# Optimization experiments

Measured on AMD Instinct MI355X. Metric: run time of the kernel, lower is better.

Reference implementation:

```python
import jax, jax.numpy as jnp
import numpy as np

DIM = 512
NUM_HEADS = 8
HEAD_DIM = DIM // NUM_HEADS
GAMMA = 1.0


def setup_inputs() -> dict:
    key = jax.random.key(0)
    ks = jax.random.split(key, 10)
    B, S = 2, 2048
    x_real = jax.random.normal(ks[0], (B, S, DIM), dtype=jnp.float32)
    x_imag = jax.random.normal(ks[1], (B, S, DIM), dtype=jnp.float32)
    def xavier(k, fan_in, fan_out):
        lim = float(np.sqrt(6.0 / (fan_in + fan_out)))
        return jax.random.uniform(k, (fan_in, fan_out), jnp.float32, -lim, lim)
    # torch Linear(in,out): weight [out,in]; we store transposed [in,out]
    Wq = xavier(ks[2], 2 * DIM, DIM); bq = jnp.zeros((DIM,), jnp.float32)
    Wk = xavier(ks[3], 2 * DIM, DIM); bk = jnp.zeros((DIM,), jnp.float32)
    Wv = xavier(ks[4], 2 * DIM, DIM); bv = jnp.zeros((DIM,), jnp.float32)
    Wo = xavier(ks[5], DIM, 2 * DIM); bo = jnp.zeros((2 * DIM,), jnp.float32)
    return {"x_real": x_real, "x_imag": x_imag, "Wq": Wq, "bq": bq,
            "Wk": Wk, "bk": bk, "Wv": Wv, "bv": bv, "Wo": Wo, "bo": bo}


def reference(x_real, x_imag, Wq, bq, Wk, bk, Wv, bv, Wo, bo):
    B, S, _ = x_real.shape
    real_embed = jnp.concatenate([x_real, x_imag], axis=-1)  # [B,S,2*dim]
    def proj(W, b):
        y = real_embed @ W + b                               # [B,S,dim]
        return y.reshape(B, S, NUM_HEADS, HEAD_DIM).transpose(0, 2, 1, 3)  # [B,H,S,d]
    Q = proj(Wq, bq)
    K = proj(Wk, bk)
    V = proj(Wv, bv)
    # softmax over head_dim is broadcast-invariant, so the Bhattacharyya
    # coefficient sum_d sqrt(p_i[d]*q_j[d]) factorizes into a matmul.
    sp = jnp.sqrt(jax.nn.softmax(Q, axis=-1))  # [B,H,S,d]
    sq = jnp.sqrt(jax.nn.softmax(K, axis=-1))  # [B,H,S,d]
    bc = jnp.einsum('bhid,bhjd->bhij', sp, sq)  # Bhattacharyya coeff [B,H,S,S]
    bc = jnp.clip(bc, -1.0, 1.0)
    dist = jnp.arccos(bc)
    attn = jax.nn.softmax(-GAMMA * dist * dist, axis=-1)  # [B,H,S,S]
    attended = jnp.einsum('bhij,bhjd->bhid', attn, V)
    attended = attended.transpose(0, 2, 1, 3).reshape(B, S, DIM)
    out = attended @ Wo + bo  # [B,S,2*dim] = concat(real_out, imag_out)
    return out
```

## Files before the change

kernel.cpp:

```cpp
#include <hip/hip_runtime.h>
#include <math.h>


typedef __attribute__((ext_vector_type(8))) short short8;
typedef __attribute__((ext_vector_type(4))) short bf16x4;
typedef __attribute__((ext_vector_type(4))) float f32x4;

#define MFMA(a, b, c) __builtin_amdgcn_mfma_f32_16x16x32_bf16((a), (b), (c), 0, 0, 0)

static __device__ __forceinline__ short f2bf(float f) {
    unsigned u = __float_as_uint(f);
    u += 0x7fffu + ((u >> 16) & 1u);
    return (short)(u >> 16);
}

static __device__ __forceinline__ void gld_lds16(const short* g, short* l) {
    __builtin_amdgcn_global_load_lds(
        (const __attribute__((address_space(1))) unsigned int*)g,
        (__attribute__((address_space(3))) unsigned int*)l, 16, 0, 0);
}

__global__ __launch_bounds__(256) void convert_x(
    const float* __restrict__ xr, const float* __restrict__ xi,
    short* __restrict__ xb)
{
    int idx = blockIdx.x * 256 + threadIdx.x;
    int e = idx << 2;
    int m = e >> 10, k = e & 1023;
    const float* src = (k < 512) ? xr : xi;
    float4 t = *(const float4*)(src + (size_t)m * 512 + (k & 511));
    unsigned lo = (unsigned short)f2bf(t.x) | ((unsigned)(unsigned short)f2bf(t.y) << 16);
    unsigned hi = (unsigned short)f2bf(t.z) | ((unsigned)(unsigned short)f2bf(t.w) << 16);
    uint2 o; o.x = lo; o.y = hi;
    *(uint2*)(xb + e) = o;
}

__global__ __launch_bounds__(256) void transpose_w(
    const float* __restrict__ Wq, const float* __restrict__ Wk,
    const float* __restrict__ Wv, const float* __restrict__ Wo,
    short* __restrict__ wqt, short* __restrict__ wkt,
    short* __restrict__ wvt, short* __restrict__ wot)
{
    __shared__ float t[32][33];
    const int z = blockIdx.z;
    const float* src = (z == 0) ? Wq : (z == 1) ? Wk : (z == 2) ? Wv : Wo;
    short* dst = (z == 0) ? wqt : (z == 1) ? wkt : (z == 2) ? wvt : wot;
    const int K = (z < 3) ? 1024 : 512;
    const int N = (z < 3) ? 512 : 1024;
    const int n0 = blockIdx.x << 5, k0 = blockIdx.y << 5;
    if (n0 >= N || k0 >= K) return;
    const int tx = threadIdx.x & 31, ty = threadIdx.x >> 5;
    #pragma unroll
    for (int i = 0; i < 4; ++i)
        t[ty + 8 * i][tx] = src[(size_t)(k0 + ty + 8 * i) * N + n0 + tx];
    __syncthreads();
    #pragma unroll
    for (int i = 0; i < 4; ++i)
        dst[(size_t)(n0 + ty + 8 * i) * K + k0 + tx] = f2bf(t[tx][ty + 8 * i]);
}

__global__ __launch_bounds__(256, 3) void qkv_mfma(
    const short* __restrict__ xb, const short* __restrict__ wcat,
    const float* __restrict__ bq, const float* __restrict__ bk,
    const float* __restrict__ bv,
    short* __restrict__ sp, short* __restrict__ sq, short* __restrict__ vt)
{
    __shared__ short As[2][128 * 32];
    __shared__ short Bs[2][128 * 32];
    const int jb = blockIdx.x;
    const int m0 = blockIdx.y << 7;
    const int tid = threadIdx.x;
    const int w = tid >> 6, lane = tid & 63;
    const int l = lane & 15, quad = lane >> 4;

    const short* gA = xb   + (size_t)(m0        + (w << 4) + (lane >> 2)) * 1024 + ((lane & 3) << 3);
    const short* gB = wcat + (size_t)((jb << 7) + (w << 4) + (lane >> 2)) * 1024 + ((lane & 3) << 3);

    gld_lds16(gA,             &As[0][w << 9]);
    gld_lds16(gA + 64 * 1024, &As[0][(w + 4) << 9]);
    gld_lds16(gB,             &Bs[0][w << 9]);
    gld_lds16(gB + 64 * 1024, &Bs[0][(w + 4) << 9]);
    __syncthreads();

    const f32x4 z4 = {0.f, 0.f, 0.f, 0.f};
    f32x4 acc[4][4];
    #pragma unroll
    for (int i = 0; i < 4; ++i)
        #pragma unroll
        for (int j = 0; j < 4; ++j) acc[i][j] = z4;

    const int rsel = (w >> 1) << 6;
    const int csel = (w & 1) << 6;

    for (int kt = 0; kt < 32; ++kt) {
        const int cb = kt & 1, nb = cb ^ 1;
        if (kt < 31) {
            const int k0 = (kt + 1) << 5;
            gld_lds16(gA + k0,             &As[nb][w << 9]);
            gld_lds16(gA + k0 + 64 * 1024, &As[nb][(w + 4) << 9]);
            gld_lds16(gB + k0,             &Bs[nb][w << 9]);
            gld_lds16(gB + k0 + 64 * 1024, &Bs[nb][(w + 4) << 9]);
        }
        const short* Al = &As[cb][rsel << 5];
        const short* Bl = &Bs[cb][csel << 5];
        short8 af[4], bfr[4];
        #pragma unroll
        for (int i = 0; i < 4; ++i)
            af[i] = *(const short8*)(Al + (((i << 4) + l) << 5) + (quad << 3));
        #pragma unroll
        for (int j = 0; j < 4; ++j)
            bfr[j] = *(const short8*)(Bl + (((j << 4) + l) << 5) + (quad << 3));
        #pragma unroll
        for (int i = 0; i < 4; ++i)
            #pragma unroll
            for (int j = 0; j < 4; ++j)
                acc[i][j] = MFMA(af[i], bfr[j], acc[i][j]);
        __syncthreads();
    }

    const int op = jb >> 2;
    const int h  = ((jb & 3) << 1) | (w & 1);

    if (op < 2) {
        short* dst = (op == 0) ? sp : sq;
        const float* bias = (op == 0) ? bq : bk;
        float bcol[4];
        #pragma unroll
        for (int nt = 0; nt < 4; ++nt) bcol[nt] = bias[(h << 6) + (nt << 4) + l];
        #pragma unroll
        for (int i = 0; i < 4; ++i) {
            #pragma unroll
            for (int reg = 0; reg < 4; ++reg) {
                const int r = m0 + rsel + (i << 4) + (quad << 2) + reg;
                const int b = r >> 11, s = r & 2047;
                float v[4];
                #pragma unroll
                for (int nt = 0; nt < 4; ++nt) v[nt] = acc[i][nt][reg] + bcol[nt];
                float mx = fmaxf(fmaxf(v[0], v[1]), fmaxf(v[2], v[3]));
                #pragma unroll
                for (int msk = 1; msk < 16; msk <<= 1) mx = fmaxf(mx, __shfl_xor(mx, msk));
                float e[4], ssum = 0.f;
                #pragma unroll
                for (int nt = 0; nt < 4; ++nt) { e[nt] = __expf(v[nt] - mx); ssum += e[nt]; }
                #pragma unroll
                for (int msk = 1; msk < 16; msk <<= 1) ssum += __shfl_xor(ssum, msk);
                float inv = 1.0f / ssum;
                short* o = dst + ((size_t)((b << 3) + h) * 2048 + s) * 64 + l;
                #pragma unroll
                for (int nt = 0; nt < 4; ++nt)
                    o[nt << 4] = f2bf(sqrtf(e[nt] * inv));
            }
        }
    } else {
        float bcol[4];
        #pragma unroll
        for (int nt = 0; nt < 4; ++nt) bcol[nt] = bv[(h << 6) + (nt << 4) + l];
        #pragma unroll
        for (int i = 0; i < 4; ++i) {
            const int sb = m0 + rsel + (i << 4) + (quad << 2);
            const int b = sb >> 11, s = sb & 2047;
            #pragma unroll
            for (int nt = 0; nt < 4; ++nt) {
                const int d = (nt << 4) + l;
                bf16x4 pk;
                #pragma unroll
                for (int reg = 0; reg < 4; ++reg)
                    pk[reg] = f2bf(acc[i][nt][reg] + bcol[nt]);
                *(bf16x4*)(vt + ((size_t)((b << 3) + h) * 64 + d) * 2048 + s) = pk;
            }
        }
    }
}

__global__ __launch_bounds__(256, 4) void attn_mfma(
    const short* __restrict__ sp, const short* __restrict__ sq,
    const short* __restrict__ vt, short* __restrict__ attB)
{
    __shared__ short sqT[2][64 * 72];
    __shared__ short vtT[2][64 * 72];
    __shared__ short Pb[4][16 * 72];
    __shared__ float denB[4][16];
    const int bh = blockIdx.y;
    const int m0 = blockIdx.x << 6;
    const int tid = threadIdx.x;
    const int w = tid >> 6, lane = tid & 63;
    const int l = lane & 15, quad = lane >> 4;

    const short* spB = sp + (size_t)bh * 2048 * 64;
    const short* sqB = sq + (size_t)bh * 2048 * 64;
    const short* vtB = vt + (size_t)bh * 64 * 2048;

    const short* apr = spB + (size_t)(m0 + w * 16 + l) * 64 + quad * 8;
    short8 aq0 = *(const short8*)(apr);
    short8 aq1 = *(const short8*)(apr + 32);

    const int srow = tid >> 2;
    const int scol = (tid & 3) * 16;
    const short* sqG = sqB + (size_t)srow * 64 + scol;
    const short* vtG = vtB + (size_t)srow * 2048 + scol;
    const int ldsOff = srow * 72 + scol;

    {
        short8 a0 = *(const short8*)(sqG);
        short8 a1 = *(const short8*)(sqG + 8);
        short8 b0 = *(const short8*)(vtG);
        short8 b1 = *(const short8*)(vtG + 8);
        *(short8*)(&sqT[0][ldsOff])     = a0;
        *(short8*)(&sqT[0][ldsOff + 8]) = a1;
        *(short8*)(&vtT[0][ldsOff])     = b0;
        *(short8*)(&vtT[0][ldsOff + 8]) = b1;
    }
    __syncthreads();

    const f32x4 z4 = {0.f, 0.f, 0.f, 0.f};
    f32x4 acc[4] = {z4, z4, z4, z4};
    float den = 0.f;
    short* Pw = &Pb[w][0];

    #pragma unroll 1
    for (int jt = 0; jt < 32; ++jt) {
        const int cb = jt & 1, nb = cb ^ 1;
        const int j0n = ((jt + 1) & 31) << 6;
        short8 na0 = *(const short8*)(sqG + (size_t)j0n * 64);
        short8 na1 = *(const short8*)(sqG + (size_t)j0n * 64 + 8);
        short8 nb0 = *(const short8*)(vtG + j0n);
        short8 nb1 = *(const short8*)(vtG + j0n + 8);

        const short* sqL = &sqT[cb][0];
        #pragma unroll
        for (int nt = 0; nt < 4; ++nt) {
            const short* ar = sqL + (nt * 16 + l) * 72 + quad * 8;
            short8 sa0 = *(const short8*)(ar);
            short8 sa1 = *(const short8*)(ar + 32);
            f32x4 p = MFMA(sa0, aq0, z4);
            p = MFMA(sa1, aq1, p);
            float wv[4];
            #pragma unroll
            for (int reg = 0; reg < 4; ++reg) {
                float u = fmaxf(1.0f - p[reg], 0.0f);
                float t = 0.000922f;
                t = fmaf(t, u, 0.00152228f);
                t = fmaf(t, u, 0.00384801f);
                t = fmaf(t, u, 0.01015873f);
                t = fmaf(t, u, 0.02857143f);
                t = fmaf(t, u, 0.08888889f);
                t = fmaf(t, u, 0.33333333f);
                t = fmaf(t, u, 2.0f);
                float e = __expf(-u * t);
                wv[reg] = e;
                den += e;
            }
            uint2 pk;
            pk.x = (__float_as_uint(wv[0]) >> 16) | (__float_as_uint(wv[1]) & 0xffff0000u);
            pk.y = (__float_as_uint(wv[2]) >> 16) | (__float_as_uint(wv[3]) & 0xffff0000u);
            *(uint2*)(&Pw[l * 72 + nt * 16 + quad * 4]) = pk;
        }

        const short* pr = Pw + l * 72 + quad * 8;
        short8 pa0 = *(const short8*)(pr);
        short8 pa1 = *(const short8*)(pr + 32);
        const short* vL = &vtT[cb][0];
        #pragma unroll
        for (int t4 = 0; t4 < 4; ++t4) {
            const short* vr = vL + (t4 * 16 + l) * 72 + quad * 8;
            short8 vb0 = *(const short8*)(vr);
            short8 vb1 = *(const short8*)(vr + 32);
            acc[t4] = MFMA(pa0, vb0, acc[t4]);
            acc[t4] = MFMA(pa1, vb1, acc[t4]);
        }

        *(short8*)(&sqT[nb][ldsOff])     = na0;
        *(short8*)(&sqT[nb][ldsOff + 8]) = na1;
        *(short8*)(&vtT[nb][ldsOff])     = nb0;
        *(short8*)(&vtT[nb][ldsOff + 8]) = nb1;
        __syncthreads();
    }

    den += __shfl_xor(den, 16);
    den += __shfl_xor(den, 32);
    if (lane < 16) denB[w][l] = den;
    float invd[4];
    #pragma unroll
    for (int reg = 0; reg < 4; ++reg)
        invd[reg] = 1.0f / denB[w][quad * 4 + reg];

    const int b = bh >> 3, hh = bh & 7;
    #pragma unroll
    for (int t4 = 0; t4 < 4; ++t4)
        #pragma unroll
        for (int reg = 0; reg < 4; ++reg) {
            const int row = m0 + w * 16 + quad * 4 + reg;
            attB[((size_t)(b * 2048 + row)) * 512 + hh * 64 + t4 * 16 + l] =
                f2bf(acc[t4][reg] * invd[reg]);
        }
}

__global__ __launch_bounds__(256, 3) void out_mfma(
    const short* __restrict__ attB, const short* __restrict__ wot,
    const float* __restrict__ bo, float* __restrict__ out)
{
    __shared__ short As[2][128 * 32];
    __shared__ short Bs[2][64 * 32];
    const int nb0 = blockIdx.x << 6;
    const int m0 = blockIdx.y << 7;
    const int tid = threadIdx.x;
    const int w = tid >> 6, lane = tid & 63;
    const int l = lane & 15, quad = lane >> 4;

    const short* gA = attB + (size_t)(m0  + (w << 4) + (lane >> 2)) * 512 + ((lane & 3) << 3);
    const short* gB = wot  + (size_t)(nb0 + (w << 4) + (lane >> 2)) * 512 + ((lane & 3) << 3);

    gld_lds16(gA,            &As[0][w << 9]);
    gld_lds16(gA + 64 * 512, &As[0][(w + 4) << 9]);
    gld_lds16(gB,            &Bs[0][w << 9]);
    __syncthreads();

    const f32x4 z4 = {0.f, 0.f, 0.f, 0.f};
    f32x4 acc[4][2];
    #pragma unroll
    for (int i = 0; i < 4; ++i) { acc[i][0] = z4; acc[i][1] = z4; }

    const int rsel = (w >> 1) << 6;
    const int csel = (w & 1) << 5;

    for (int kt = 0; kt < 16; ++kt) {
        const int cb = kt & 1, nbuf = cb ^ 1;
        if (kt < 15) {
            const int k0 = (kt + 1) << 5;
            gld_lds16(gA + k0,            &As[nbuf][w << 9]);
            gld_lds16(gA + k0 + 64 * 512, &As[nbuf][(w + 4) << 9]);
            gld_lds16(gB + k0,            &Bs[nbuf][w << 9]);
        }
        const short* Al = &As[cb][rsel << 5];
        const short* Bl = &Bs[cb][csel << 5];
        short8 af[4], bfr[2];
        #pragma unroll
        for (int i = 0; i < 4; ++i)
            af[i] = *(const short8*)(Al + (((i << 4) + l) << 5) + (quad << 3));
        #pragma unroll
        for (int j = 0; j < 2; ++j)
            bfr[j] = *(const short8*)(Bl + (((j << 4) + l) << 5) + (quad << 3));
        #pragma unroll
        for (int i = 0; i < 4; ++i) {
            acc[i][0] = MFMA(af[i], bfr[0], acc[i][0]);
            acc[i][1] = MFMA(af[i], bfr[1], acc[i][1]);
        }
        __syncthreads();
    }

    const int n0 = nb0 + csel;
    float bcol[2];
    bcol[0] = bo[n0 + l];
    bcol[1] = bo[n0 + 16 + l];
    #pragma unroll
    for (int i = 0; i < 4; ++i)
        #pragma unroll
        for (int reg = 0; reg < 4; ++reg) {
            const int m = m0 + rsel + (i << 4) + (quad << 2) + reg;
            float* o = out + (size_t)m * 1024 + n0 + l;
            o[0]  = acc[i][0][reg] + bcol[0];
            o[16] = acc[i][1][reg] + bcol[1];
        }
}

extern "C" void kernel_launch(void* const* d_in, const int* in_sizes, int n_in,
                              void* d_out, int out_size, void* d_ws, size_t ws_size,
                              hipStream_t stream) {
    const float* xr = (const float*)d_in[0];
    const float* xi = (const float*)d_in[1];
    const float* Wq = (const float*)d_in[2];
    const float* bq = (const float*)d_in[3];
    const float* Wk = (const float*)d_in[4];
    const float* bk = (const float*)d_in[5];
    const float* Wv = (const float*)d_in[6];
    const float* bv = (const float*)d_in[7];
    const float* Wo = (const float*)d_in[8];
    const float* bo = (const float*)d_in[9];
    float* out = (float*)d_out;

    short* base = (short*)d_ws;
    short* xb   = base;
    short* wqt  = xb  + 4194304;
    short* wkt  = wqt + 524288;
    short* wvt  = wkt + 524288;
    short* wot  = wvt + 524288;
    short* spW  = wot + 524288;
    short* sqW  = spW + 2097152;
    short* vtW  = sqW + 2097152;
    short* attB = vtW + 2097152;

    hipLaunchKernelGGL(convert_x, dim3(4096), dim3(256), 0, stream, xr, xi, xb);
    hipLaunchKernelGGL(transpose_w, dim3(32, 32, 4), dim3(256), 0, stream,
                       Wq, Wk, Wv, Wo, wqt, wkt, wvt, wot);
    hipLaunchKernelGGL(qkv_mfma, dim3(12, 32), dim3(256), 0, stream,
                       xb, wqt, bq, bk, bv, spW, sqW, vtW);
    hipLaunchKernelGGL(attn_mfma, dim3(32, 16), dim3(256), 0, stream,
                       spW, sqW, vtW, attB);
    hipLaunchKernelGGL(out_mfma, dim3(16, 32), dim3(256), 0, stream,
                       attB, wot, bo, out);
}
```

Baseline: 184.7 us.

## Retile QKV projection to 128x64 blocks of two waves for more blocks

```diff
diff --git a/kernel.cpp b/kernel.cpp
--- a/kernel.cpp
+++ b/kernel.cpp
@@ -59,27 +59,31 @@
         dst[(size_t)(n0 + ty + 8 * i) * K + k0 + tx] = f2bf(t[tx][ty + 8 * i]);
 }
 
-__global__ __launch_bounds__(256, 3) void qkv_mfma(
+__global__ __launch_bounds__(128, 4) void qkv_mfma(
     const short* __restrict__ xb, const short* __restrict__ wcat,
     const float* __restrict__ bq, const float* __restrict__ bk,
     const float* __restrict__ bv,
     short* __restrict__ sp, short* __restrict__ sq, short* __restrict__ vt)
 {
     __shared__ short As[2][128 * 32];
-    __shared__ short Bs[2][128 * 32];
+    __shared__ short Bs[2][64 * 32];
     const int jb = blockIdx.x;
     const int m0 = blockIdx.y << 7;
     const int tid = threadIdx.x;
     const int w = tid >> 6, lane = tid & 63;
     const int l = lane & 15, quad = lane >> 4;
 
-    const short* gA = xb   + (size_t)(m0        + (w << 4) + (lane >> 2)) * 1024 + ((lane & 3) << 3);
-    const short* gB = wcat + (size_t)((jb << 7) + (w << 4) + (lane >> 2)) * 1024 + ((lane & 3) << 3);
-
-    gld_lds16(gA,             &As[0][w << 9]);
-    gld_lds16(gA + 64 * 1024, &As[0][(w + 4) << 9]);
-    gld_lds16(gB,             &Bs[0][w << 9]);
-    gld_lds16(gB + 64 * 1024, &Bs[0][(w + 4) << 9]);
+    const int srow = lane >> 2;
+    const int sseg = (lane & 3) << 3;
+    const short* gA = xb   + (size_t)(m0        + (w << 6) + srow) * 1024 + sseg;
+    const short* gB = wcat + (size_t)((jb << 6) + (w << 5) + srow) * 1024 + sseg;
+
+    #pragma unroll
+    for (int t = 0; t < 4; ++t)
+        gld_lds16(gA + t * 16 * 1024, &As[0][((w << 2) + t) << 9]);
+    #pragma unroll
+    for (int t = 0; t < 2; ++t)
+        gld_lds16(gB + t * 16 * 1024, &Bs[0][((w << 1) + t) << 9]);
     __syncthreads();
 
     const f32x4 z4 = {0.f, 0.f, 0.f, 0.f};
@@ -88,21 +92,20 @@
     for (int i = 0; i < 4; ++i)
         #pragma unroll
         for (int j = 0; j < 4; ++j) acc[i][j] = z4;
-
-    const int rsel = (w >> 1) << 6;
-    const int csel = (w & 1) << 6;
 
     for (int kt = 0; kt < 32; ++kt) {
         const int cb = kt & 1, nb = cb ^ 1;
         if (kt < 31) {
             const int k0 = (kt + 1) << 5;
-            gld_lds16(gA + k0,             &As[nb][w << 9]);
-            gld_lds16(gA + k0 + 64 * 1024, &As[nb][(w + 4) << 9]);
-            gld_lds16(gB + k0,             &Bs[nb][w << 9]);
-            gld_lds16(gB + k0 + 64 * 1024, &Bs[nb][(w + 4) << 9]);
-        }
-        const short* Al = &As[cb][rsel << 5];
-        const short* Bl = &Bs[cb][csel << 5];
+            #pragma unroll
+            for (int t = 0; t < 4; ++t)
+                gld_lds16(gA + k0 + t * 16 * 1024, &As[nb][((w << 2) + t) << 9]);
+            #pragma unroll
+            for (int t = 0; t < 2; ++t)
+                gld_lds16(gB + k0 + t * 16 * 1024, &Bs[nb][((w << 1) + t) << 9]);
+        }
+        const short* Al = &As[cb][(w << 6) << 5];
+        const short* Bl = &Bs[cb][0];
         short8 af[4], bfr[4];
         #pragma unroll
         for (int i = 0; i < 4; ++i)
@@ -118,8 +121,8 @@
         __syncthreads();
     }
 
-    const int op = jb >> 2;
-    const int h  = ((jb & 3) << 1) | (w & 1);
+    const int op = jb >> 3;
+    const int h  = jb & 7;
 
     if (op < 2) {
         short* dst = (op == 0) ? sp : sq;
@@ -131,7 +134,7 @@
         for (int i = 0; i < 4; ++i) {
             #pragma unroll
             for (int reg = 0; reg < 4; ++reg) {
-                const int r = m0 + rsel + (i << 4) + (quad << 2) + reg;
+                const int r = m0 + (w << 6) + (i << 4) + (quad << 2) + reg;
                 const int b = r >> 11, s = r & 2047;
                 float v[4];
                 #pragma unroll
@@ -157,7 +160,7 @@
         for (int nt = 0; nt < 4; ++nt) bcol[nt] = bv[(h << 6) + (nt << 4) + l];
         #pragma unroll
         for (int i = 0; i < 4; ++i) {
-            const int sb = m0 + rsel + (i << 4) + (quad << 2);
+            const int sb = m0 + (w << 6) + (i << 4) + (quad << 2);
             const int b = sb >> 11, s = sb & 2047;
             #pragma unroll
             for (int nt = 0; nt < 4; ++nt) {
@@ -392,7 +395,7 @@
     hipLaunchKernelGGL(convert_x, dim3(4096), dim3(256), 0, stream, xr, xi, xb);
     hipLaunchKernelGGL(transpose_w, dim3(32, 32, 4), dim3(256), 0, stream,
                        Wq, Wk, Wv, Wo, wqt, wkt, wvt, wot);
-    hipLaunchKernelGGL(qkv_mfma, dim3(12, 32), dim3(256), 0, stream,
+    hipLaunchKernelGGL(qkv_mfma, dim3(24, 32), dim3(128), 0, stream,
                        xb, wqt, bq, bk, bv, spW, sqW, vtW);
     hipLaunchKernelGGL(attn_mfma, dim3(32, 16), dim3(256), 0, stream,
                        spW, sqW, vtW, attB);
```

After: 189.1 us. 1.02x slower.
